# Performance work log

Hardware: AMD Instinct MI355X
Metric: run time of the kernel (lower is better)

The kernel has to match this reference:

```python
import jax, jax.numpy as jnp
import numpy as np

L = 32        # label_num = len(label2idx)
SOS = 0       # label2idx['[SOS]']
END = 1       # label2idx['[END]']
NEG = -10000.0
B, T = 512, 1024


def setup_inputs() -> dict:
    key = jax.random.key(0)
    k1, k2, k3 = jax.random.split(key, 3)
    emission = jax.random.normal(k1, (B, T, L), dtype=jnp.float32)
    label_ids = jax.random.randint(k2, (B, T), 0, L)
    transitions = jax.random.normal(k3, (L, L), dtype=jnp.float32)
    # CrfLayer.__init__: forbid transitions into [SOS] and out of [END]
    transitions = transitions.at[SOS, :].set(NEG).at[:, END].set(NEG)
    return {"emission": emission, "label_ids": label_ids, "transitions": transitions}


def reference(emission, label_ids, transitions):
    b, t, l = emission.shape
    # ---- _forward_alg: log-partition via sequential logsumexp recurrence ----
    alpha0 = jnp.full((b, l), NEG, dtype=emission.dtype).at[:, SOS].set(0.0)
    feats_t = jnp.transpose(emission, (1, 0, 2))  # [T, B, L]

    def step(alpha, feat):
        # aa[b, j, i] = alpha[b, i] + feat[b, j] + transitions[j, i]
        aa = alpha[:, None, :] + feat[:, :, None] + transitions[None, :, :]
        return jax.nn.logsumexp(aa, axis=2), None

    alpha, _ = jax.lax.scan(step, alpha0, feats_t)
    forward_score = jax.nn.logsumexp(alpha + transitions[END][None, :], axis=1)  # [B]

    # ---- _score_sentence: score of the gold path ----
    tags = jnp.concatenate(
        [jnp.full((b, 1), SOS, dtype=label_ids.dtype), label_ids], axis=1)  # [B, T+1]
    trans_score = transitions[tags[:, 1:], tags[:, :-1]].sum(axis=1)          # [B]
    emit_score = jnp.take_along_axis(
        emission, tags[:, 1:, None].astype(jnp.int32), axis=2)[..., 0].sum(axis=1)  # [B]
    gold_score = trans_score + emit_score + transitions[END, tags[:, -1]]

    # loss = sum(forward_score - gold_score)
    return jnp.sum(forward_score - gold_score)
```

## Files before the change

kernel.cpp:

```cpp
#include <hip/hip_runtime.h>


typedef float    f32x16 __attribute__((ext_vector_type(16)));
typedef short    s16x8  __attribute__((ext_vector_type(8)));
typedef unsigned u32x2  __attribute__((ext_vector_type(2)));

#define TT 1024
#define LL 32
#define BB 512
#define NC 16
#define CL 64
#define MS 33

#if __has_builtin(__builtin_amdgcn_permlane32_swap)
#define HAVE_PLSWAP 1
#else
#define HAVE_PLSWAP 0
#endif

union Frag { s16x8 v; unsigned u[4]; };

__device__ __forceinline__ unsigned pack_bf16(float lo, float hi) {
    return __builtin_amdgcn_perm(__float_as_uint(hi), __float_as_uint(lo), 0x07060302u);
}

__global__ __launch_bounds__(NC * 64, 8) void crf_fused_kernel(
    const float* __restrict__ emission,
    const int*   __restrict__ label_ids,
    const float* __restrict__ transitions,
    float*       __restrict__ out)
{
    __shared__ __align__(16) float shM[NC][32 * MS];
    __shared__ float shQ[2][64];
    __shared__ float emitArr[NC], tgArr[NC];
    __shared__ int   capArr[NC];

    const int tid  = threadIdx.x;
    const int w    = tid >> 6;
    const int lane = tid & 63;
    const int j    = lane & 31;
    const int h    = lane >> 5;
    const int b    = blockIdx.x;
    const int t0   = w * CL;

    const int*   labB = label_ids + b * TT + t0;
    const float* emB  = emission + ((size_t)b * TT + t0) * LL + j;

    {
        int t  = t0 + lane;
        int l1 = labB[lane];
        int l0 = (t == 0) ? 0 : label_ids[b * TT + t - 1];
        float tg = transitions[(l1 << 5) + l0];
        if (t == TT - 1) tg += transitions[32 + l1];
#pragma unroll
        for (int m = 32; m >= 1; m >>= 1) tg += __shfl_xor(tg, m, 64);
        if (lane == 0) tgArr[w] = tg;
    }

    const float* trow = transitions + j * 32;
    float E0[8], E1[8];
#pragma unroll
    for (int i = 0; i < 8; ++i) {
        E0[i] = __expf(trow[8 * h + i]);
        E1[i] = __expf(trow[16 + 8 * h + i]);
    }

    Frag B0, B1;
#pragma unroll
    for (int i = 0; i < 8; ++i) {
        B0.v[i] = (short)((8 * h + i == j) ? 0x3F80 : 0);
        B1.v[i] = (short)((16 + 8 * h + i == j) ? 0x3F80 : 0);
    }

    f32x16 zc, acc;
#pragma unroll
    for (int i = 0; i < 16; ++i) zc[i] = 0.0f;

    float ring[8];
#pragma unroll
    for (int s = 0; s < 8; ++s) ring[s] = emB[s * LL];

    float sc = 1.0f;
    int   Cap = 0, ep1 = 0, ep2 = 0;
    float emit = 0.0f;

#pragma unroll 8
    for (int s = 0; s < CL; ++s) {
        float feat = ring[s & 7];
        int   lab  = labB[s];
        emit += (j == lab) ? feat : 0.0f;
        float fs = __expf(feat) * sc;

        Frag A0, A1;
#pragma unroll
        for (int p = 0; p < 4; ++p) {
            A0.u[p] = pack_bf16(fs * E0[2 * p], fs * E0[2 * p + 1]);
            A1.u[p] = pack_bf16(fs * E1[2 * p], fs * E1[2 * p + 1]);
        }

        acc = __builtin_amdgcn_mfma_f32_32x32x16_bf16(A0.v, B0.v, zc, 0, 0, 0);
        acc = __builtin_amdgcn_mfma_f32_32x32x16_bf16(A1.v, B1.v, acc, 0, 0, 0);

        int pb = __builtin_amdgcn_readlane(__float_as_int(acc[2]), 0);
        int e  = ((pb >> 23) & 0xff) - 127;
        sc = __int_as_float((127 - ep1) << 23);
        Cap += e;
        ep2 = ep1; ep1 = e;

        int nf = s + 8; nf = (nf < CL) ? nf : (CL - 1);
        ring[s & 7] = emB[nf * LL];

#if HAVE_PLSWAP
        {
            u32x2 p0 = __builtin_amdgcn_permlane32_swap(__float_as_uint(acc[0]),  __float_as_uint(acc[4]),  false, false);
            u32x2 p1 = __builtin_amdgcn_permlane32_swap(__float_as_uint(acc[1]),  __float_as_uint(acc[5]),  false, false);
            u32x2 p2 = __builtin_amdgcn_permlane32_swap(__float_as_uint(acc[2]),  __float_as_uint(acc[6]),  false, false);
            u32x2 p3 = __builtin_amdgcn_permlane32_swap(__float_as_uint(acc[3]),  __float_as_uint(acc[7]),  false, false);
            B0.u[0] = pack_bf16(__uint_as_float(p0[0]), __uint_as_float(p1[0]));
            B0.u[1] = pack_bf16(__uint_as_float(p2[0]), __uint_as_float(p3[0]));
            B0.u[2] = pack_bf16(__uint_as_float(p0[1]), __uint_as_float(p1[1]));
            B0.u[3] = pack_bf16(__uint_as_float(p2[1]), __uint_as_float(p3[1]));
            u32x2 q0 = __builtin_amdgcn_permlane32_swap(__float_as_uint(acc[8]),  __float_as_uint(acc[12]), false, false);
            u32x2 q1 = __builtin_amdgcn_permlane32_swap(__float_as_uint(acc[9]),  __float_as_uint(acc[13]), false, false);
            u32x2 q2 = __builtin_amdgcn_permlane32_swap(__float_as_uint(acc[10]), __float_as_uint(acc[14]), false, false);
            u32x2 q3 = __builtin_amdgcn_permlane32_swap(__float_as_uint(acc[11]), __float_as_uint(acc[15]), false, false);
            B1.u[0] = pack_bf16(__uint_as_float(q0[0]), __uint_as_float(q1[0]));
            B1.u[1] = pack_bf16(__uint_as_float(q2[0]), __uint_as_float(q3[0]));
            B1.u[2] = pack_bf16(__uint_as_float(q0[1]), __uint_as_float(q1[1]));
            B1.u[3] = pack_bf16(__uint_as_float(q2[1]), __uint_as_float(q3[1]));
        }
#else
        {
            const int swaddr = (lane ^ 32) << 2;
            float sw[16];
#pragma unroll
            for (int r = 0; r < 16; ++r)
                sw[r] = __int_as_float(
                    __builtin_amdgcn_ds_bpermute(swaddr, __float_as_int(acc[r])));
            float b0v[8], b1v[8];
#pragma unroll
            for (int i = 0; i < 4; ++i) {
                b0v[i]     = h ? sw[4 + i]   : acc[i];
                b0v[4 + i] = h ? acc[4 + i]  : sw[i];
                b1v[i]     = h ? sw[12 + i]  : acc[8 + i];
                b1v[4 + i] = h ? acc[12 + i] : sw[8 + i];
            }
#pragma unroll
            for (int p = 0; p < 4; ++p) {
                B0.u[p] = pack_bf16(b0v[2 * p], b0v[2 * p + 1]);
                B1.u[p] = pack_bf16(b1v[2 * p], b1v[2 * p + 1]);
            }
        }
#endif
    }
    Cap -= (ep1 + ep2);

#pragma unroll
    for (int r = 0; r < 16; ++r) {
        int row = (r & 3) + 8 * (r >> 2) + 4 * h;
        shM[w][row * MS + j] = acc[r];
    }
#pragma unroll
    for (int m = 16; m >= 1; m >>= 1) emit += __shfl_xor(emit, m, 32);
    if (lane == 0) { emitArr[w] = emit; capArr[w] = Cap; }

    __syncthreads();

    if (w == 0) {
        const float Eend = __expf(transitions[32 + j]);
        float q = (j == 0) ? 1.0f : 0.0f;
        int   Cq = 0;
        float emitT = 0.0f;

#pragma unroll
        for (int c = 0; c < NC; ++c) {
            shQ[c & 1][lane] = q;
            asm volatile("s_waitcnt lgkmcnt(0)" ::: "memory");
            __builtin_amdgcn_wave_barrier();
            const float* Mrow = &shM[c][j * MS];
            const float* qv   = &shQ[c & 1][h * 32];
            float a0 = 0.f, a1 = 0.f, a2 = 0.f, a3 = 0.f;
#pragma unroll
            for (int i = 0; i < 32; i += 4) {
                a0 = fmaf(Mrow[i],     qv[i],     a0);
                a1 = fmaf(Mrow[i + 1], qv[i + 1], a1);
                a2 = fmaf(Mrow[i + 2], qv[i + 2], a2);
                a3 = fmaf(Mrow[i + 3], qv[i + 3], a3);
            }
            float qn = (a0 + a1) + (a2 + a3);
            int pb = __builtin_amdgcn_readlane(__float_as_int(qn), 2);
            int e  = ((pb >> 23) & 0xff) - 127;
            qn *= __int_as_float((127 - e) << 23);
            Cq += e + capArr[c];
            emitT += emitArr[c];
            q = qn;
        }

        float v = q * Eend;
#pragma unroll
        for (int m = 16; m >= 1; m >>= 1) v += __shfl_xor(v, m, 32);
        float fwd = __logf(v) + (float)Cq * 0.69314718055994531f;

        float tgold = 0.0f;
#pragma unroll
        for (int c = 0; c < NC; ++c) tgold += tgArr[c];

        if (lane == 0) atomicAdd(out, fwd - emitT - tgold);
    }
}

extern "C" void kernel_launch(void* const* d_in, const int* in_sizes, int n_in,
                              void* d_out, int out_size, void* d_ws, size_t ws_size,
                              hipStream_t stream)
{
    const float* emission    = (const float*)d_in[0];
    const int*   label_ids   = (const int*)d_in[1];
    const float* transitions = (const float*)d_in[2];
    float* out = (float*)d_out;

    hipMemsetAsync(out, 0, sizeof(float), stream);
    crf_fused_kernel<<<BB, NC * 64, 0, stream>>>(emission, label_ids, transitions, out);
}
```

Measured before the change: 161.6 us.

## Permute state index order to drop cross-half swaps and rescale every fourth step

Reorders the label indices used by the transition exponent table and the identity B fragment so the MFMA accumulator layout directly matches the next step's B operand. This removes the per-step permlane32 swap or bpermute exchange. Renormalisation now happens once every four steps instead of every step. Gold-path emission gathering moves from the per-step loop into a prologue gather. Chunks become 8 waves of 128 steps instead of 16 of 64, which halves the serial merge work but also halves the wave-level parallelism per block. Skipping rescales for three steps risks bf16/fp32 overflow or precision drift.

Result: faster. 137.5 us (-14.9%).

```diff
diff --git a/kernel.cpp b/kernel.cpp
--- a/kernel.cpp
+++ b/kernel.cpp
@@ -1,22 +1,15 @@
 #include <hip/hip_runtime.h>
 
 
-typedef float    f32x16 __attribute__((ext_vector_type(16)));
-typedef short    s16x8  __attribute__((ext_vector_type(8)));
-typedef unsigned u32x2  __attribute__((ext_vector_type(2)));
+typedef float  f32x16 __attribute__((ext_vector_type(16)));
+typedef short  s16x8  __attribute__((ext_vector_type(8)));
 
 #define TT 1024
 #define LL 32
 #define BB 512
-#define NC 16
-#define CL 64
+#define NC 8
+#define CL 128
 #define MS 33
-
-#if __has_builtin(__builtin_amdgcn_permlane32_swap)
-#define HAVE_PLSWAP 1
-#else
-#define HAVE_PLSWAP 0
-#endif
 
 union Frag { s16x8 v; unsigned u[4]; };
 
@@ -24,7 +17,7 @@
     return __builtin_amdgcn_perm(__float_as_uint(hi), __float_as_uint(lo), 0x07060302u);
 }
 
-__global__ __launch_bounds__(NC * 64, 8) void crf_fused_kernel(
+__global__ __launch_bounds__(NC * 64, 4) void crf_fused_kernel(
     const float* __restrict__ emission,
     const int*   __restrict__ label_ids,
     const float* __restrict__ transitions,
@@ -32,7 +25,7 @@
 {
     __shared__ __align__(16) float shM[NC][32 * MS];
     __shared__ float shQ[2][64];
-    __shared__ float emitArr[NC], tgArr[NC];
+    __shared__ float tgArr[NC];
     __shared__ int   capArr[NC];
 
     const int tid  = threadIdx.x;
@@ -47,29 +40,36 @@
     const float* emB  = emission + ((size_t)b * TT + t0) * LL + j;
 
     {
-        int t  = t0 + lane;
-        int l1 = labB[lane];
-        int l0 = (t == 0) ? 0 : label_ids[b * TT + t - 1];
-        float tg = transitions[(l1 << 5) + l0];
-        if (t == TT - 1) tg += transitions[32 + l1];
+        float g = 0.0f;
 #pragma unroll
-        for (int m = 32; m >= 1; m >>= 1) tg += __shfl_xor(tg, m, 64);
-        if (lane == 0) tgArr[w] = tg;
+        for (int u = 0; u < 2; ++u) {
+            int tt = t0 + 64 * u + lane;
+            int l1 = labB[64 * u + lane];
+            int l0 = (tt == 0) ? 0 : label_ids[b * TT + tt - 1];
+            g += transitions[(l1 << 5) + l0];
+            g += emission[((size_t)b * TT + tt) * LL + l1];
+            if (tt == TT - 1) g += transitions[32 + l1];
+        }
+#pragma unroll
+        for (int m = 32; m >= 1; m >>= 1) g += __shfl_xor(g, m, 64);
+        if (lane == 0) tgArr[w] = g;
     }
 
     const float* trow = transitions + j * 32;
     float E0[8], E1[8];
 #pragma unroll
     for (int i = 0; i < 8; ++i) {
-        E0[i] = __expf(trow[8 * h + i]);
-        E1[i] = __expf(trow[16 + 8 * h + i]);
+        int col = (i & 3) + 8 * (i >> 2) + 4 * h;
+        E0[i] = __expf(trow[col]);
+        E1[i] = __expf(trow[16 + col]);
     }
 
     Frag B0, B1;
 #pragma unroll
     for (int i = 0; i < 8; ++i) {
-        B0.v[i] = (short)((8 * h + i == j) ? 0x3F80 : 0);
-        B1.v[i] = (short)((16 + 8 * h + i == j) ? 0x3F80 : 0);
+        int row = (i & 3) + 8 * (i >> 2) + 4 * h;
+        B0.v[i] = (short)((row == j)      ? 0x3F80 : 0);
+        B1.v[i] = (short)((row + 16 == j) ? 0x3F80 : 0);
     }
 
     f32x16 zc, acc;
@@ -81,88 +81,52 @@
     for (int s = 0; s < 8; ++s) ring[s] = emB[s * LL];
 
     float sc = 1.0f;
-    int   Cap = 0, ep1 = 0, ep2 = 0;
-    float emit = 0.0f;
+    int   Cap = 0, elast = 0;
 
-#pragma unroll 8
-    for (int s = 0; s < CL; ++s) {
-        float feat = ring[s & 7];
-        int   lab  = labB[s];
-        emit += (j == lab) ? feat : 0.0f;
-        float fs = __expf(feat) * sc;
+    for (int s0 = 0; s0 < CL; s0 += 8) {
+#pragma unroll
+        for (int k = 0; k < 8; ++k) {
+            const int s = s0 + k;
+            float feat = ring[k];
 
-        Frag A0, A1;
-#pragma unroll
-        for (int p = 0; p < 4; ++p) {
-            A0.u[p] = pack_bf16(fs * E0[2 * p], fs * E0[2 * p + 1]);
-            A1.u[p] = pack_bf16(fs * E1[2 * p], fs * E1[2 * p + 1]);
-        }
+            float fs = ((k & 3) == 0) ? (__expf(feat) * sc) : __expf(feat);
 
-        acc = __builtin_amdgcn_mfma_f32_32x32x16_bf16(A0.v, B0.v, zc, 0, 0, 0);
-        acc = __builtin_amdgcn_mfma_f32_32x32x16_bf16(A1.v, B1.v, acc, 0, 0, 0);
-
-        int pb = __builtin_amdgcn_readlane(__float_as_int(acc[2]), 0);
-        int e  = ((pb >> 23) & 0xff) - 127;
-        sc = __int_as_float((127 - ep1) << 23);
-        Cap += e;
-        ep2 = ep1; ep1 = e;
-
-        int nf = s + 8; nf = (nf < CL) ? nf : (CL - 1);
-        ring[s & 7] = emB[nf * LL];
-
-#if HAVE_PLSWAP
-        {
-            u32x2 p0 = __builtin_amdgcn_permlane32_swap(__float_as_uint(acc[0]),  __float_as_uint(acc[4]),  false, false);
-            u32x2 p1 = __builtin_amdgcn_permlane32_swap(__float_as_uint(acc[1]),  __float_as_uint(acc[5]),  false, false);
-            u32x2 p2 = __builtin_amdgcn_permlane32_swap(__float_as_uint(acc[2]),  __float_as_uint(acc[6]),  false, false);
-            u32x2 p3 = __builtin_amdgcn_permlane32_swap(__float_as_uint(acc[3]),  __float_as_uint(acc[7]),  false, false);
-            B0.u[0] = pack_bf16(__uint_as_float(p0[0]), __uint_as_float(p1[0]));
-            B0.u[1] = pack_bf16(__uint_as_float(p2[0]), __uint_as_float(p3[0]));
-            B0.u[2] = pack_bf16(__uint_as_float(p0[1]), __uint_as_float(p1[1]));
-            B0.u[3] = pack_bf16(__uint_as_float(p2[1]), __uint_as_float(p3[1]));
-            u32x2 q0 = __builtin_amdgcn_permlane32_swap(__float_as_uint(acc[8]),  __float_as_uint(acc[12]), false, false);
-            u32x2 q1 = __builtin_amdgcn_permlane32_swap(__float_as_uint(acc[9]),  __float_as_uint(acc[13]), false, false);
-            u32x2 q2 = __builtin_amdgcn_permlane32_swap(__float_as_uint(acc[10]), __float_as_uint(acc[14]), false, false);
-            u32x2 q3 = __builtin_amdgcn_permlane32_swap(__float_as_uint(acc[11]), __float_as_uint(acc[15]), false, false);
-            B1.u[0] = pack_bf16(__uint_as_float(q0[0]), __uint_as_float(q1[0]));
-            B1.u[1] = pack_bf16(__uint_as_float(q2[0]), __uint_as_float(q3[0]));
-            B1.u[2] = pack_bf16(__uint_as_float(q0[1]), __uint_as_float(q1[1]));
-            B1.u[3] = pack_bf16(__uint_as_float(q2[1]), __uint_as_float(q3[1]));
-        }
-#else
-        {
-            const int swaddr = (lane ^ 32) << 2;
-            float sw[16];
-#pragma unroll
-            for (int r = 0; r < 16; ++r)
-                sw[r] = __int_as_float(
-                    __builtin_amdgcn_ds_bpermute(swaddr, __float_as_int(acc[r])));
-            float b0v[8], b1v[8];
-#pragma unroll
-            for (int i = 0; i < 4; ++i) {
-                b0v[i]     = h ? sw[4 + i]   : acc[i];
-                b0v[4 + i] = h ? acc[4 + i]  : sw[i];
-                b1v[i]     = h ? sw[12 + i]  : acc[8 + i];
-                b1v[4 + i] = h ? acc[12 + i] : sw[8 + i];
-            }
+            Frag A0, A1;
 #pragma unroll
             for (int p = 0; p < 4; ++p) {
-                B0.u[p] = pack_bf16(b0v[2 * p], b0v[2 * p + 1]);
-                B1.u[p] = pack_bf16(b1v[2 * p], b1v[2 * p + 1]);
+                A0.u[p] = pack_bf16(fs * E0[2 * p], fs * E0[2 * p + 1]);
+                A1.u[p] = pack_bf16(fs * E1[2 * p], fs * E1[2 * p + 1]);
+            }
+
+            acc = __builtin_amdgcn_mfma_f32_32x32x16_bf16(A0.v, B0.v, zc, 0, 0, 0);
+            acc = __builtin_amdgcn_mfma_f32_32x32x16_bf16(A1.v, B1.v, acc, 0, 0, 0);
+
+            if ((k & 3) == 3) {
+                int pb = __builtin_amdgcn_readlane(__float_as_int(acc[2]), 0);
+                int e  = ((pb >> 23) & 0xff) - 127;
+                sc = __int_as_float((127 - e) << 23);
+                Cap += e;
+                elast = e;
+            }
+
+            int nf = s + 8; nf = (nf < CL) ? nf : (CL - 1);
+            ring[k] = emB[nf * LL];
+
+#pragma unroll
+            for (int p = 0; p < 4; ++p) {
+                B0.u[p] = pack_bf16(acc[2 * p],     acc[2 * p + 1]);
+                B1.u[p] = pack_bf16(acc[8 + 2 * p], acc[9 + 2 * p]);
             }
         }
-#endif
     }
-    Cap -= (ep1 + ep2);
+    Cap -= elast;
 
 #pragma unroll
     for (int r = 0; r < 16; ++r) {
         int row = (r & 3) + 8 * (r >> 2) + 4 * h;
         shM[w][row * MS + j] = acc[r];
     }
-#pragma unroll
-    for (int m = 16; m >= 1; m >>= 1) emit += __shfl_xor(emit, m, 32);
-    if (lane == 0) { emitArr[w] = emit; capArr[w] = Cap; }
+    if (lane == 0) capArr[w] = Cap;
 
     __syncthreads();
 
@@ -170,7 +134,7 @@
         const float Eend = __expf(transitions[32 + j]);
         float q = (j == 0) ? 1.0f : 0.0f;
         int   Cq = 0;
-        float emitT = 0.0f;
+        float gold = 0.0f;
 
 #pragma unroll
         for (int c = 0; c < NC; ++c) {
@@ -192,7 +156,7 @@
             int e  = ((pb >> 23) & 0xff) - 127;
             qn *= __int_as_float((127 - e) << 23);
             Cq += e + capArr[c];
-            emitT += emitArr[c];
+            gold += tgArr[c];
             q = qn;
         }
 
@@ -201,11 +165,7 @@
         for (int m = 16; m >= 1; m >>= 1) v += __shfl_xor(v, m, 32);
         float fwd = __logf(v) + (float)Cq * 0.69314718055994531f;
 
-        float tgold = 0.0f;
-#pragma unroll
-        for (int c = 0; c < NC; ++c) tgold += tgArr[c];
-
-        if (lane == 0) atomicAdd(out, fwd - emitT - tgold);
+        if (lane == 0) atomicAdd(out, fwd - gold);
     }
 }
 
```
